# Performance work log

Hardware: AMD Instinct MI355X
Metric: run time of the kernel (lower is better)

Reference implementation:

```python
import jax, jax.numpy as jnp
import numpy as np

B, D, N = 256, 256, 100000
NUM_CLUSTERS, NUM_CLASSES = 100, 1000


def setup_inputs() -> dict:
    key = jax.random.key(0)
    k1, k2, k3, k4, k5, k6 = jax.random.split(key, 6)
    return {
        "feature": jax.random.normal(k1, (B, D), dtype=jnp.float32),
        "feature_bank": jax.random.normal(k2, (N, D), dtype=jnp.float32),
        "cluster_label_bank": jax.random.randint(k3, (N,), 0, NUM_CLUSTERS, dtype=jnp.int64)
            if jax.config.jax_enable_x64 else jax.random.randint(k3, (N,), 0, NUM_CLUSTERS).astype(jnp.int32),
        "class_label_bank": jax.random.randint(k4, (N,), 0, NUM_CLASSES).astype(jnp.int32),
        "cluster_idx": jax.random.randint(k5, (B,), 0, NUM_CLUSTERS).astype(jnp.int32),
        "gt_label": jax.random.randint(k6, (B,), 0, NUM_CLASSES).astype(jnp.int32),
    }


def reference(feature, feature_bank, cluster_label_bank, class_label_bank, cluster_idx, gt_label):
    # Masks: primary = same cluster AND different class; fallback = different class only.
    cluster_label_bank = cluster_label_bank.astype(jnp.int32)
    same_cluster = cluster_label_bank[None, :] == cluster_idx[:, None].astype(jnp.int32)  # [B, N]
    diff_class = class_label_bank[None, :] != gt_label[:, None]                            # [B, N]
    mask_primary = same_cluster & diff_class
    has_primary = mask_primary.any(axis=1, keepdims=True)
    mask = jnp.where(has_primary, mask_primary, diff_class)  # [B, N]

    # Euclidean distances (torch.cdist p=2): ||a-b|| via expanded squared form.
    a2 = jnp.sum(feature * feature, axis=1)[:, None]              # [B, 1]
    b2 = jnp.sum(feature_bank * feature_bank, axis=1)[None, :]    # [1, N]
    d2 = a2 + b2 - 2.0 * (feature @ feature_bank.T)               # [B, N]
    dist = jnp.sqrt(jnp.maximum(d2, 0.0))

    # Masked argmin over the bank, then gather negatives.
    dist_masked = jnp.where(mask, dist, jnp.inf)
    neg_idx = jnp.argmin(dist_masked, axis=1)                     # [B]
    negatives = feature_bank[neg_idx]                             # [B, D]
    return negatives
```

## Files before the change

kernel.cpp:

```cpp
#include <hip/hip_runtime.h>
#include <climits>

typedef __attribute__((ext_vector_type(8))) short s8;
typedef __attribute__((ext_vector_type(4))) float f32x4;

#define BQ    256
#define DDIM  256
#define NBANK 100000
#define BN    64
#define NJB   ((NBANK + BN - 1) / BN)
#define SENT  1e30f

__device__ inline void splitElem(float x, s8& h, s8& l, int i) {
    unsigned u  = __float_as_uint(x);
    unsigned uh = (u + 0x8000u) & 0xFFFF0000u;
    h[i] = (short)(uh >> 16);
    float lf = x - __uint_as_float(uh);
    l[i] = (short)((__float_as_uint(lf) + 0x8000u) >> 16);
}

__device__ inline void split8(const float4 v0, const float4 v1, s8& h, s8& l) {
    splitElem(v0.x, h, l, 0); splitElem(v0.y, h, l, 1);
    splitElem(v0.z, h, l, 2); splitElem(v0.w, h, l, 3);
    splitElem(v1.x, h, l, 4); splitElem(v1.y, h, l, 5);
    splitElem(v1.z, h, l, 6); splitElem(v1.w, h, l, 7);
}

__device__ inline float sq8(const float4 v0, const float4 v1, float s) {
    s = fmaf(v0.x, v0.x, s); s = fmaf(v0.y, v0.y, s);
    s = fmaf(v0.z, v0.z, s); s = fmaf(v0.w, v0.w, s);
    s = fmaf(v1.x, v1.x, s); s = fmaf(v1.y, v1.y, s);
    s = fmaf(v1.z, v1.z, s); s = fmaf(v1.w, v1.w, s);
    return s;
}

__device__ inline unsigned fkey(float f) {
    unsigned u = __float_as_uint(f);
    return u ^ (((int)u < 0) ? 0xFFFFFFFFu : 0x80000000u);
}

__global__ __launch_bounds__(512) void split_feature(
    const float* __restrict__ feature, s8* __restrict__ fH, s8* __restrict__ fL)
{
    const int t    = blockIdx.x * 512 + threadIdx.x;
    const int lane = t & 63, ks = (t >> 6) & 7, rt = t >> 9;
    const int row  = rt * 16 + (lane & 15);
    const int k0   = ks * 32 + (lane >> 4) * 8;
    const float* p = feature + (size_t)row * DDIM + k0;
    const float4 v0 = *(const float4*)p;
    const float4 v1 = *(const float4*)(p + 4);
    s8 h, l;
    split8(v0, v1, h, l);
    fH[t] = h; fL[t] = l;
}

__global__ __launch_bounds__(512, 4) void gemm_argmin_msplit(
    const s8* __restrict__ fH, const s8* __restrict__ fL,
    const float* __restrict__ bank,
    const int* __restrict__ cluster_label, const int* __restrict__ class_label,
    const int* __restrict__ cluster_idx,  const int* __restrict__ gt_label,
    unsigned long long* __restrict__ wsP, unsigned long long* __restrict__ wsD)
{
    __shared__ __align__(16) s8 bHs[4 * 4 * 64];
    __shared__ __align__(16) s8 bLs[4 * 4 * 64];
    __shared__ float b2s[BN];
    __shared__ int clsS[BN], cluS[BN], rowGt[128], rowClu[128];

    const int tid = threadIdx.x;
    const int bb  = blockIdx.x;
    const int jb  = bb >> 1, mh = bb & 1;
    const int j0  = jb * BN;
    const int r0  = mh * 128;

    const int col = tid >> 3, q = tid & 7;
    const int ct_s = col >> 4, cl_s = col & 15;
    const int sl_s = q >> 1, p_s = q & 1;
    const int w = tid >> 6, lane = tid & 63;
    const int g = lane >> 4, c = lane & 15;

    int jcol = j0 + col; if (jcol >= NBANK) jcol = NBANK - 1;
    const float* gb = bank + (size_t)jcol * DDIM + q * 16;

    if (tid < 128) {
        rowGt[tid]  = gt_label[r0 + tid];
        rowClu[tid] = cluster_idx[r0 + tid];
    }
    if (tid < BN) {
        int jg = j0 + tid; int jc = jg < NBANK ? jg : NBANK - 1;
        clsS[tid] = class_label[jc];
        cluS[tid] = cluster_label[jc];
    }
    float4 a0 = *(const float4*)(gb);
    float4 a1 = *(const float4*)(gb + 4);
    float4 a2 = *(const float4*)(gb + 8);
    float4 a3 = *(const float4*)(gb + 12);

    float sqa = 0.f;
    {
        s8 h, l;
        split8(a0, a1, h, l);
        sqa = sq8(a0, a1, sqa);
        int wi = (((sl_s * 4 + ct_s) * 64 + (p_s * 2 + 0) * 16 + cl_s)) ^ q;
        bHs[wi] = h; bLs[wi] = l;
        split8(a2, a3, h, l);
        sqa = sq8(a2, a3, sqa);
        wi = (((sl_s * 4 + ct_s) * 64 + (p_s * 2 + 1) * 16 + cl_s)) ^ q;
        bHs[wi] = h; bLs[wi] = l;
    }
    __syncthreads();

    a0 = *(const float4*)(gb + 128);
    a1 = *(const float4*)(gb + 132);
    a2 = *(const float4*)(gb + 136);
    a3 = *(const float4*)(gb + 140);

    f32x4 acc[4];
    #pragma unroll
    for (int ct = 0; ct < 4; ++ct)
        acc[ct] = (f32x4){0.f, 0.f, 0.f, 0.f};

    const int RT = mh * 8 + w;

    #pragma unroll
    for (int sl = 0; sl < 4; ++sl) {
        const s8 aH = fH[(RT * 8 + sl) * 64 + lane];
        const s8 aL = fL[(RT * 8 + sl) * 64 + lane];
        const int rx = sl * 2 + (lane >> 5);
        #pragma unroll
        for (int ct = 0; ct < 4; ++ct) {
            const s8 bh = bHs[((sl * 4 + ct) * 64 + lane) ^ rx];
            const s8 bl = bLs[((sl * 4 + ct) * 64 + lane) ^ rx];
            acc[ct] = __builtin_amdgcn_mfma_f32_16x16x32_bf16(aH, bh, acc[ct], 0, 0, 0);
            acc[ct] = __builtin_amdgcn_mfma_f32_16x16x32_bf16(aH, bl, acc[ct], 0, 0, 0);
            acc[ct] = __builtin_amdgcn_mfma_f32_16x16x32_bf16(aL, bh, acc[ct], 0, 0, 0);
        }
    }
    __syncthreads();

    {
        s8 h, l;
        split8(a0, a1, h, l);
        sqa = sq8(a0, a1, sqa);
        int wi = (((sl_s * 4 + ct_s) * 64 + (p_s * 2 + 0) * 16 + cl_s)) ^ q;
        bHs[wi] = h; bLs[wi] = l;
        split8(a2, a3, h, l);
        sqa = sq8(a2, a3, sqa);
        wi = (((sl_s * 4 + ct_s) * 64 + (p_s * 2 + 1) * 16 + cl_s)) ^ q;
        bHs[wi] = h; bLs[wi] = l;
    }
    sqa += __shfl_xor(sqa, 1);
    sqa += __shfl_xor(sqa, 2);
    sqa += __shfl_xor(sqa, 4);
    if (q == 0) b2s[col] = sqa;
    __syncthreads();

    #pragma unroll
    for (int sl = 0; sl < 4; ++sl) {
        const s8 aH = fH[(RT * 8 + 4 + sl) * 64 + lane];
        const s8 aL = fL[(RT * 8 + 4 + sl) * 64 + lane];
        const int rx = sl * 2 + (lane >> 5);
        #pragma unroll
        for (int ct = 0; ct < 4; ++ct) {
            const s8 bh = bHs[((sl * 4 + ct) * 64 + lane) ^ rx];
            const s8 bl = bLs[((sl * 4 + ct) * 64 + lane) ^ rx];
            acc[ct] = __builtin_amdgcn_mfma_f32_16x16x32_bf16(aH, bh, acc[ct], 0, 0, 0);
            acc[ct] = __builtin_amdgcn_mfma_f32_16x16x32_bf16(aH, bl, acc[ct], 0, 0, 0);
            acc[ct] = __builtin_amdgcn_mfma_f32_16x16x32_bf16(aL, bh, acc[ct], 0, 0, 0);
        }
    }

    #pragma unroll
    for (int r = 0; r < 4; ++r) {
        const int lrow = w * 16 + g * 4 + r;
        const int myGt = rowGt[lrow], myClu = rowClu[lrow];
        unsigned long long pk = ~0ull, dk = ~0ull;
        #pragma unroll
        for (int ct = 0; ct < 4; ++ct) {
            const int jg = j0 + ct * 16 + c;
            const float sc = b2s[ct * 16 + c] - 2.f * acc[ct][r];
            if (jg < NBANK && clsS[ct * 16 + c] != myGt) {
                const unsigned long long k =
                    ((unsigned long long)fkey(sc) << 32) | (unsigned)jg;
                dk = k < dk ? k : dk;
                if (cluS[ct * 16 + c] == myClu) pk = k < pk ? k : pk;
            }
        }
        #pragma unroll
        for (int off = 1; off < 16; off <<= 1) {
            unsigned long long ok = __shfl_xor(pk, off);
            pk = ok < pk ? ok : pk;
            ok = __shfl_xor(dk, off);
            dk = ok < dk ? ok : dk;
        }
        if (c == 0) {
            const size_t o = (size_t)jb * BQ + r0 + lrow;
            wsP[o] = pk;
            wsD[o] = dk;
        }
    }
}

__global__ __launch_bounds__(256) void reduce_gather(
    const unsigned long long* __restrict__ wsP,
    const unsigned long long* __restrict__ wsD,
    const float* __restrict__ bank, float* __restrict__ out)
{
    const int row = blockIdx.x, tid = threadIdx.x;
    unsigned long long pk = ~0ull, dk = ~0ull;
    for (int b = tid; b < NJB; b += 256) {
        unsigned long long k = wsP[(size_t)b * BQ + row];
        pk = k < pk ? k : pk;
        k = wsD[(size_t)b * BQ + row];
        dk = k < dk ? k : dk;
    }
    #pragma unroll
    for (int off = 32; off > 0; off >>= 1) {
        unsigned long long ok = __shfl_down(pk, off);
        pk = ok < pk ? ok : pk;
        ok = __shfl_down(dk, off);
        dk = ok < dk ? ok : dk;
    }
    __shared__ unsigned long long swP[4], swD[4];
    __shared__ int sIdx;
    const int lane = tid & 63, wv = tid >> 6;
    if (lane == 0) { swP[wv] = pk; swD[wv] = dk; }
    __syncthreads();
    if (tid == 0) {
        unsigned long long p = swP[0], d = swD[0];
        #pragma unroll
        for (int k2 = 1; k2 < 4; ++k2) {
            p = swP[k2] < p ? swP[k2] : p;
            d = swD[k2] < d ? swD[k2] : d;
        }
        sIdx = (p != ~0ull) ? (int)(unsigned)(p & 0xFFFFFFFFull)
             : ((d != ~0ull) ? (int)(unsigned)(d & 0xFFFFFFFFull) : 0);
    }
    __syncthreads();
    out[(size_t)row * DDIM + tid] = bank[(size_t)sIdx * DDIM + tid];
}

extern "C" void kernel_launch(void* const* d_in, const int* in_sizes, int n_in,
                              void* d_out, int out_size, void* d_ws, size_t ws_size,
                              hipStream_t stream) {
    const float* feature       = (const float*)d_in[0];
    const float* bank          = (const float*)d_in[1];
    const int*   cluster_label = (const int*)d_in[2];
    const int*   class_label   = (const int*)d_in[3];
    const int*   cluster_idx   = (const int*)d_in[4];
    const int*   gt_label      = (const int*)d_in[5];
    float* out = (float*)d_out;

    s8* fH = (s8*)d_ws;
    s8* fL = fH + 8192;
    unsigned long long* wsP = (unsigned long long*)((char*)d_ws + 2 * 8192 * sizeof(s8));
    unsigned long long* wsD = wsP + (size_t)BQ * NJB;

    hipLaunchKernelGGL(split_feature, dim3(16), dim3(512), 0, stream, feature, fH, fL);
    hipLaunchKernelGGL(gemm_argmin_msplit, dim3(NJB * 2), dim3(512), 0, stream,
                       fH, fL, bank, cluster_label, class_label, cluster_idx, gt_label,
                       wsP, wsD);
    hipLaunchKernelGGL(reduce_gather, dim3(BQ), dim3(256), 0, stream,
                       wsP, wsD, bank, out);
}
```

Before: 217.8 us.

## Process two bank column tiles per block with cross-tile prefetch

Each GEMM block now handles 128 bank columns as two consecutive 64-column tiles instead of one. The global loads for the next tile are issued before the current tile's MFMA work, so memory latency overlaps compute across tile boundaries. This also halves the number of blocks and the partial-result workspace that the reduction kernel scans. The cost is longer serial work per block and fewer blocks, which may reduce load balance across CUs.

```diff
diff --git a/kernel.cpp b/kernel.cpp
--- a/kernel.cpp
+++ b/kernel.cpp
@@ -9,6 +9,7 @@
 #define NBANK 100000
 #define BN    64
 #define NJB   ((NBANK + BN - 1) / BN)
+#define NJB2  ((NJB + 1) / 2)
 #define SENT  1e30f
 
 __device__ inline void splitElem(float x, s8& h, s8& l, int i) {
@@ -54,7 +55,7 @@
     fH[t] = h; fL[t] = l;
 }
 
-__global__ __launch_bounds__(512, 4) void gemm_argmin_msplit(
+__global__ __launch_bounds__(512, 4) void gemm_argmin_2t(
     const s8* __restrict__ fH, const s8* __restrict__ fL,
     const float* __restrict__ bank,
     const int* __restrict__ cluster_label, const int* __restrict__ class_label,
@@ -63,13 +64,13 @@
 {
     __shared__ __align__(16) s8 bHs[4 * 4 * 64];
     __shared__ __align__(16) s8 bLs[4 * 4 * 64];
-    __shared__ float b2s[BN];
-    __shared__ int clsS[BN], cluS[BN], rowGt[128], rowClu[128];
+    __shared__ float b2s[128];
+    __shared__ int clsS[128], cluS[128], rowGt[128], rowClu[128];
 
     const int tid = threadIdx.x;
     const int bb  = blockIdx.x;
-    const int jb  = bb >> 1, mh = bb & 1;
-    const int j0  = jb * BN;
+    const int jb2 = bb >> 1, mh = bb & 1;
+    const int j0  = jb2 * 128;
     const int r0  = mh * 128;
 
     const int col = tid >> 3, q = tid & 7;
@@ -77,98 +78,83 @@
     const int sl_s = q >> 1, p_s = q & 1;
     const int w = tid >> 6, lane = tid & 63;
     const int g = lane >> 4, c = lane & 15;
-
-    int jcol = j0 + col; if (jcol >= NBANK) jcol = NBANK - 1;
-    const float* gb = bank + (size_t)jcol * DDIM + q * 16;
+    const int RT = mh * 8 + w;
+
+    int jc0 = j0 + col;      if (jc0 >= NBANK) jc0 = NBANK - 1;
+    int jc1 = j0 + 64 + col; if (jc1 >= NBANK) jc1 = NBANK - 1;
+    const float* gb0 = bank + (size_t)jc0 * DDIM + q * 16;
+    const float* gb1 = bank + (size_t)jc1 * DDIM + q * 16;
 
     if (tid < 128) {
         rowGt[tid]  = gt_label[r0 + tid];
         rowClu[tid] = cluster_idx[r0 + tid];
-    }
-    if (tid < BN) {
         int jg = j0 + tid; int jc = jg < NBANK ? jg : NBANK - 1;
         clsS[tid] = class_label[jc];
         cluS[tid] = cluster_label[jc];
     }
-    float4 a0 = *(const float4*)(gb);
-    float4 a1 = *(const float4*)(gb + 4);
-    float4 a2 = *(const float4*)(gb + 8);
-    float4 a3 = *(const float4*)(gb + 12);
+    float4 a0 = *(const float4*)(gb0);
+    float4 a1 = *(const float4*)(gb0 + 4);
+    float4 a2 = *(const float4*)(gb0 + 8);
+    float4 a3 = *(const float4*)(gb0 + 12);
+
+#define STAGE(SQA)                                                             \
+    {                                                                          \
+        s8 h_, l_;                                                             \
+        split8(a0, a1, h_, l_);                                                \
+        SQA = sq8(a0, a1, SQA);                                                \
+        int wi_ = (((sl_s * 4 + ct_s) * 64 + (p_s * 2 + 0) * 16 + cl_s)) ^ q;  \
+        bHs[wi_] = h_; bLs[wi_] = l_;                                          \
+        split8(a2, a3, h_, l_);                                                \
+        SQA = sq8(a2, a3, SQA);                                                \
+        wi_ = (((sl_s * 4 + ct_s) * 64 + (p_s * 2 + 1) * 16 + cl_s)) ^ q;      \
+        bHs[wi_] = h_; bLs[wi_] = l_;                                          \
+    }
+
+#define LOADA(PTR, OFF)                                                        \
+    a0 = *(const float4*)((PTR) + (OFF));                                      \
+    a1 = *(const float4*)((PTR) + (OFF) + 4);                                  \
+    a2 = *(const float4*)((PTR) + (OFF) + 8);                                  \
+    a3 = *(const float4*)((PTR) + (OFF) + 12);
+
+#define COMPUTE(HBASE)                                                         \
+    _Pragma("unroll")                                                          \
+    for (int sl = 0; sl < 4; ++sl) {                                           \
+        const s8 aH = fH[(RT * 8 + (HBASE) + sl) * 64 + lane];                 \
+        const s8 aL = fL[(RT * 8 + (HBASE) + sl) * 64 + lane];                 \
+        const int rx = sl * 2 + (lane >> 5);                                   \
+        _Pragma("unroll")                                                      \
+        for (int ct = 0; ct < 4; ++ct) {                                       \
+            const s8 bh = bHs[((sl * 4 + ct) * 64 + lane) ^ rx];               \
+            const s8 bl = bLs[((sl * 4 + ct) * 64 + lane) ^ rx];               \
+            acc[ct] = __builtin_amdgcn_mfma_f32_16x16x32_bf16(aH, bh, acc[ct], 0, 0, 0); \
+            acc[ct] = __builtin_amdgcn_mfma_f32_16x16x32_bf16(aH, bl, acc[ct], 0, 0, 0); \
+            acc[ct] = __builtin_amdgcn_mfma_f32_16x16x32_bf16(aL, bh, acc[ct], 0, 0, 0); \
+        }                                                                      \
+    }
+
+    f32x4 acc[4];
+    unsigned long long pkA[4], dkA[4];
 
     float sqa = 0.f;
-    {
-        s8 h, l;
-        split8(a0, a1, h, l);
-        sqa = sq8(a0, a1, sqa);
-        int wi = (((sl_s * 4 + ct_s) * 64 + (p_s * 2 + 0) * 16 + cl_s)) ^ q;
-        bHs[wi] = h; bLs[wi] = l;
-        split8(a2, a3, h, l);
-        sqa = sq8(a2, a3, sqa);
-        wi = (((sl_s * 4 + ct_s) * 64 + (p_s * 2 + 1) * 16 + cl_s)) ^ q;
-        bHs[wi] = h; bLs[wi] = l;
-    }
-    __syncthreads();
-
-    a0 = *(const float4*)(gb + 128);
-    a1 = *(const float4*)(gb + 132);
-    a2 = *(const float4*)(gb + 136);
-    a3 = *(const float4*)(gb + 140);
-
-    f32x4 acc[4];
-    #pragma unroll
-    for (int ct = 0; ct < 4; ++ct)
-        acc[ct] = (f32x4){0.f, 0.f, 0.f, 0.f};
-
-    const int RT = mh * 8 + w;
-
-    #pragma unroll
-    for (int sl = 0; sl < 4; ++sl) {
-        const s8 aH = fH[(RT * 8 + sl) * 64 + lane];
-        const s8 aL = fL[(RT * 8 + sl) * 64 + lane];
-        const int rx = sl * 2 + (lane >> 5);
-        #pragma unroll
-        for (int ct = 0; ct < 4; ++ct) {
-            const s8 bh = bHs[((sl * 4 + ct) * 64 + lane) ^ rx];
-            const s8 bl = bLs[((sl * 4 + ct) * 64 + lane) ^ rx];
-            acc[ct] = __builtin_amdgcn_mfma_f32_16x16x32_bf16(aH, bh, acc[ct], 0, 0, 0);
-            acc[ct] = __builtin_amdgcn_mfma_f32_16x16x32_bf16(aH, bl, acc[ct], 0, 0, 0);
-            acc[ct] = __builtin_amdgcn_mfma_f32_16x16x32_bf16(aL, bh, acc[ct], 0, 0, 0);
-        }
-    }
-    __syncthreads();
-
-    {
-        s8 h, l;
-        split8(a0, a1, h, l);
-        sqa = sq8(a0, a1, sqa);
-        int wi = (((sl_s * 4 + ct_s) * 64 + (p_s * 2 + 0) * 16 + cl_s)) ^ q;
-        bHs[wi] = h; bLs[wi] = l;
-        split8(a2, a3, h, l);
-        sqa = sq8(a2, a3, sqa);
-        wi = (((sl_s * 4 + ct_s) * 64 + (p_s * 2 + 1) * 16 + cl_s)) ^ q;
-        bHs[wi] = h; bLs[wi] = l;
-    }
+    STAGE(sqa);
+    __syncthreads();
+    LOADA(gb0, 128);
+    #pragma unroll
+    for (int ct = 0; ct < 4; ++ct) acc[ct] = (f32x4){0.f, 0.f, 0.f, 0.f};
+    COMPUTE(0);
+    __syncthreads();
+    STAGE(sqa);
     sqa += __shfl_xor(sqa, 1);
     sqa += __shfl_xor(sqa, 2);
     sqa += __shfl_xor(sqa, 4);
     if (q == 0) b2s[col] = sqa;
     __syncthreads();
-
-    #pragma unroll
-    for (int sl = 0; sl < 4; ++sl) {
-        const s8 aH = fH[(RT * 8 + 4 + sl) * 64 + lane];
-        const s8 aL = fL[(RT * 8 + 4 + sl) * 64 + lane];
-        const int rx = sl * 2 + (lane >> 5);
-        #pragma unroll
-        for (int ct = 0; ct < 4; ++ct) {
-            const s8 bh = bHs[((sl * 4 + ct) * 64 + lane) ^ rx];
-            const s8 bl = bLs[((sl * 4 + ct) * 64 + lane) ^ rx];
-            acc[ct] = __builtin_amdgcn_mfma_f32_16x16x32_bf16(aH, bh, acc[ct], 0, 0, 0);
-            acc[ct] = __builtin_amdgcn_mfma_f32_16x16x32_bf16(aH, bl, acc[ct], 0, 0, 0);
-            acc[ct] = __builtin_amdgcn_mfma_f32_16x16x32_bf16(aL, bh, acc[ct], 0, 0, 0);
-        }
-    }
-
+    LOADA(gb1, 0);
+    COMPUTE(4);
+    __syncthreads();
+
+    sqa = 0.f;
+    STAGE(sqa);
     #pragma unroll
     for (int r = 0; r < 4; ++r) {
         const int lrow = w * 16 + g * 4 + r;
@@ -176,13 +162,48 @@
         unsigned long long pk = ~0ull, dk = ~0ull;
         #pragma unroll
         for (int ct = 0; ct < 4; ++ct) {
-            const int jg = j0 + ct * 16 + c;
-            const float sc = b2s[ct * 16 + c] - 2.f * acc[ct][r];
-            if (jg < NBANK && clsS[ct * 16 + c] != myGt) {
+            const int li = ct * 16 + c;
+            const int jg = j0 + li;
+            const float sc = b2s[li] - 2.f * acc[ct][r];
+            if (jg < NBANK && clsS[li] != myGt) {
                 const unsigned long long k =
                     ((unsigned long long)fkey(sc) << 32) | (unsigned)jg;
                 dk = k < dk ? k : dk;
-                if (cluS[ct * 16 + c] == myClu) pk = k < pk ? k : pk;
+                if (cluS[li] == myClu) pk = k < pk ? k : pk;
+            }
+        }
+        pkA[r] = pk; dkA[r] = dk;
+    }
+    __syncthreads();
+
+    LOADA(gb1, 128);
+    #pragma unroll
+    for (int ct = 0; ct < 4; ++ct) acc[ct] = (f32x4){0.f, 0.f, 0.f, 0.f};
+    COMPUTE(0);
+    __syncthreads();
+    STAGE(sqa);
+    sqa += __shfl_xor(sqa, 1);
+    sqa += __shfl_xor(sqa, 2);
+    sqa += __shfl_xor(sqa, 4);
+    if (q == 0) b2s[64 + col] = sqa;
+    __syncthreads();
+    COMPUTE(4);
+
+    #pragma unroll
+    for (int r = 0; r < 4; ++r) {
+        const int lrow = w * 16 + g * 4 + r;
+        const int myGt = rowGt[lrow], myClu = rowClu[lrow];
+        unsigned long long pk = pkA[r], dk = dkA[r];
+        #pragma unroll
+        for (int ct = 0; ct < 4; ++ct) {
+            const int li = 64 + ct * 16 + c;
+            const int jg = j0 + li;
+            const float sc = b2s[li] - 2.f * acc[ct][r];
+            if (jg < NBANK && clsS[li] != myGt) {
+                const unsigned long long k =
+                    ((unsigned long long)fkey(sc) << 32) | (unsigned)jg;
+                dk = k < dk ? k : dk;
+                if (cluS[li] == myClu) pk = k < pk ? k : pk;
             }
         }
         #pragma unroll
@@ -193,11 +214,14 @@
             dk = ok < dk ? ok : dk;
         }
         if (c == 0) {
-            const size_t o = (size_t)jb * BQ + r0 + lrow;
+            const size_t o = (size_t)jb2 * BQ + r0 + lrow;
             wsP[o] = pk;
             wsD[o] = dk;
         }
     }
+#undef STAGE
+#undef LOADA
+#undef COMPUTE
 }
 
 __global__ __launch_bounds__(256) void reduce_gather(
@@ -207,7 +231,7 @@
 {
     const int row = blockIdx.x, tid = threadIdx.x;
     unsigned long long pk = ~0ull, dk = ~0ull;
-    for (int b = tid; b < NJB; b += 256) {
+    for (int b = tid; b < NJB2; b += 256) {
         unsigned long long k = wsP[(size_t)b * BQ + row];
         pk = k < pk ? k : pk;
         k = wsD[(size_t)b * BQ + row];
@@ -253,10 +277,10 @@
     s8* fH = (s8*)d_ws;
     s8* fL = fH + 8192;
     unsigned long long* wsP = (unsigned long long*)((char*)d_ws + 2 * 8192 * sizeof(s8));
-    unsigned long long* wsD = wsP + (size_t)BQ * NJB;
+    unsigned long long* wsD = wsP + (size_t)BQ * NJB2;
 
     hipLaunchKernelGGL(split_feature, dim3(16), dim3(512), 0, stream, feature, fH, fL);
-    hipLaunchKernelGGL(gemm_argmin_msplit, dim3(NJB * 2), dim3(512), 0, stream,
+    hipLaunchKernelGGL(gemm_argmin_2t, dim3(NJB2 * 2), dim3(512), 0, stream,
                        fH, fL, bank, cluster_label, class_label, cluster_idx, gt_label,
                        wsP, wsD);
     hipLaunchKernelGGL(reduce_gather, dim3(BQ), dim3(256), 0, stream,
```

Result: no change. 214.9 us (-1.3%).

## Cover all 256 query rows per block with 1024 threads instead of splitting M

Applied to the files above, without the earlier changes.

Each block previously handled half of the query rows, so every bank tile was loaded from global memory, split into bf16 hi/lo and squared twice, once per M-half. Now one 1024-thread block covers all 256 rows for its 64-column bank tile, so each bank element is loaded and converted only once, with each thread handling 8 floats per phase. The cost is fewer, larger blocks: occupancy limits under launch_bounds(1024,4) and fewer independent blocks to hide latency may offset the halved bank traffic.

```diff
diff --git a/kernel.cpp b/kernel.cpp
--- a/kernel.cpp
+++ b/kernel.cpp
@@ -54,7 +54,7 @@
     fH[t] = h; fL[t] = l;
 }
 
-__global__ __launch_bounds__(512, 4) void gemm_argmin_msplit(
+__global__ __launch_bounds__(1024, 4) void gemm_argmin_fullm(
     const s8* __restrict__ fH, const s8* __restrict__ fL,
     const float* __restrict__ bank,
     const int* __restrict__ cluster_label, const int* __restrict__ class_label,
@@ -64,26 +64,24 @@
     __shared__ __align__(16) s8 bHs[4 * 4 * 64];
     __shared__ __align__(16) s8 bLs[4 * 4 * 64];
     __shared__ float b2s[BN];
-    __shared__ int clsS[BN], cluS[BN], rowGt[128], rowClu[128];
+    __shared__ int clsS[BN], cluS[BN], rowGt[BQ], rowClu[BQ];
 
     const int tid = threadIdx.x;
-    const int bb  = blockIdx.x;
-    const int jb  = bb >> 1, mh = bb & 1;
+    const int jb  = blockIdx.x;
     const int j0  = jb * BN;
-    const int r0  = mh * 128;
-
-    const int col = tid >> 3, q = tid & 7;
+
+    const int col = tid >> 4, q = tid & 15;
     const int ct_s = col >> 4, cl_s = col & 15;
-    const int sl_s = q >> 1, p_s = q & 1;
+    const int sl_s = q >> 2, o_s = q & 3;
     const int w = tid >> 6, lane = tid & 63;
     const int g = lane >> 4, c = lane & 15;
 
     int jcol = j0 + col; if (jcol >= NBANK) jcol = NBANK - 1;
-    const float* gb = bank + (size_t)jcol * DDIM + q * 16;
-
-    if (tid < 128) {
-        rowGt[tid]  = gt_label[r0 + tid];
-        rowClu[tid] = cluster_idx[r0 + tid];
+    const float* gb = bank + (size_t)jcol * DDIM + q * 8;
+
+    if (tid < BQ) {
+        rowGt[tid]  = gt_label[tid];
+        rowClu[tid] = cluster_idx[tid];
     }
     if (tid < BN) {
         int jg = j0 + tid; int jc = jg < NBANK ? jg : NBANK - 1;
@@ -92,40 +90,30 @@
     }
     float4 a0 = *(const float4*)(gb);
     float4 a1 = *(const float4*)(gb + 4);
-    float4 a2 = *(const float4*)(gb + 8);
-    float4 a3 = *(const float4*)(gb + 12);
 
     float sqa = 0.f;
     {
         s8 h, l;
         split8(a0, a1, h, l);
         sqa = sq8(a0, a1, sqa);
-        int wi = (((sl_s * 4 + ct_s) * 64 + (p_s * 2 + 0) * 16 + cl_s)) ^ q;
-        bHs[wi] = h; bLs[wi] = l;
-        split8(a2, a3, h, l);
-        sqa = sq8(a2, a3, sqa);
-        wi = (((sl_s * 4 + ct_s) * 64 + (p_s * 2 + 1) * 16 + cl_s)) ^ q;
+        const int wi = (((sl_s * 4 + ct_s) * 64 + o_s * 16 + cl_s)) ^ q;
         bHs[wi] = h; bLs[wi] = l;
     }
     __syncthreads();
 
     a0 = *(const float4*)(gb + 128);
     a1 = *(const float4*)(gb + 132);
-    a2 = *(const float4*)(gb + 136);
-    a3 = *(const float4*)(gb + 140);
 
     f32x4 acc[4];
     #pragma unroll
     for (int ct = 0; ct < 4; ++ct)
         acc[ct] = (f32x4){0.f, 0.f, 0.f, 0.f};
 
-    const int RT = mh * 8 + w;
-
     #pragma unroll
     for (int sl = 0; sl < 4; ++sl) {
-        const s8 aH = fH[(RT * 8 + sl) * 64 + lane];
-        const s8 aL = fL[(RT * 8 + sl) * 64 + lane];
-        const int rx = sl * 2 + (lane >> 5);
+        const s8 aH = fH[(w * 8 + sl) * 64 + lane];
+        const s8 aL = fL[(w * 8 + sl) * 64 + lane];
+        const int rx = sl * 4 + g;
         #pragma unroll
         for (int ct = 0; ct < 4; ++ct) {
             const s8 bh = bHs[((sl * 4 + ct) * 64 + lane) ^ rx];
@@ -141,24 +129,21 @@
         s8 h, l;
         split8(a0, a1, h, l);
         sqa = sq8(a0, a1, sqa);
-        int wi = (((sl_s * 4 + ct_s) * 64 + (p_s * 2 + 0) * 16 + cl_s)) ^ q;
-        bHs[wi] = h; bLs[wi] = l;
-        split8(a2, a3, h, l);
-        sqa = sq8(a2, a3, sqa);
-        wi = (((sl_s * 4 + ct_s) * 64 + (p_s * 2 + 1) * 16 + cl_s)) ^ q;
+        const int wi = (((sl_s * 4 + ct_s) * 64 + o_s * 16 + cl_s)) ^ q;
         bHs[wi] = h; bLs[wi] = l;
     }
     sqa += __shfl_xor(sqa, 1);
     sqa += __shfl_xor(sqa, 2);
     sqa += __shfl_xor(sqa, 4);
+    sqa += __shfl_xor(sqa, 8);
     if (q == 0) b2s[col] = sqa;
     __syncthreads();
 
     #pragma unroll
     for (int sl = 0; sl < 4; ++sl) {
-        const s8 aH = fH[(RT * 8 + 4 + sl) * 64 + lane];
-        const s8 aL = fL[(RT * 8 + 4 + sl) * 64 + lane];
-        const int rx = sl * 2 + (lane >> 5);
+        const s8 aH = fH[(w * 8 + 4 + sl) * 64 + lane];
+        const s8 aL = fL[(w * 8 + 4 + sl) * 64 + lane];
+        const int rx = sl * 4 + g;
         #pragma unroll
         for (int ct = 0; ct < 4; ++ct) {
             const s8 bh = bHs[((sl * 4 + ct) * 64 + lane) ^ rx];
@@ -171,18 +156,19 @@
 
     #pragma unroll
     for (int r = 0; r < 4; ++r) {
-        const int lrow = w * 16 + g * 4 + r;
-        const int myGt = rowGt[lrow], myClu = rowClu[lrow];
+        const int row  = w * 16 + g * 4 + r;
+        const int myGt = rowGt[row], myClu = rowClu[row];
         unsigned long long pk = ~0ull, dk = ~0ull;
         #pragma unroll
         for (int ct = 0; ct < 4; ++ct) {
-            const int jg = j0 + ct * 16 + c;
-            const float sc = b2s[ct * 16 + c] - 2.f * acc[ct][r];
-            if (jg < NBANK && clsS[ct * 16 + c] != myGt) {
+            const int li = ct * 16 + c;
+            const int jg = j0 + li;
+            const float sc = b2s[li] - 2.f * acc[ct][r];
+            if (jg < NBANK && clsS[li] != myGt) {
                 const unsigned long long k =
                     ((unsigned long long)fkey(sc) << 32) | (unsigned)jg;
                 dk = k < dk ? k : dk;
-                if (cluS[ct * 16 + c] == myClu) pk = k < pk ? k : pk;
+                if (cluS[li] == myClu) pk = k < pk ? k : pk;
             }
         }
         #pragma unroll
@@ -193,7 +179,7 @@
             dk = ok < dk ? ok : dk;
         }
         if (c == 0) {
-            const size_t o = (size_t)jb * BQ + r0 + lrow;
+            const size_t o = (size_t)jb * BQ + row;
             wsP[o] = pk;
             wsD[o] = dk;
         }
@@ -256,7 +242,7 @@
     unsigned long long* wsD = wsP + (size_t)BQ * NJB;
 
     hipLaunchKernelGGL(split_feature, dim3(16), dim3(512), 0, stream, feature, fH, fL);
-    hipLaunchKernelGGL(gemm_argmin_msplit, dim3(NJB * 2), dim3(512), 0, stream,
+    hipLaunchKernelGGL(gemm_argmin_fullm, dim3(NJB), dim3(1024), 0, stream,
                        fH, fL, bank, cluster_label, class_label, cluster_idx, gt_label,
                        wsP, wsD);
     hipLaunchKernelGGL(reduce_gather, dim3(BQ), dim3(256), 0, stream,
```

Measured after the change: 218.2 us. No clear change (+0.2%).

## Cover all 256 query rows per block so each bank tile is split once

Applied to the files above, without the earlier changes.

Drops the two-way split over query rows. Each block now processes all 256 feature rows against its 64-column bank tile, with every wave computing two 16-row tiles. Before, the two row halves each loaded the same bank tile from global memory and converted it to bf16 hi/lo, so this removes that duplicated load and split work and halves the grid. In exchange each wave holds twice the accumulators, which raises register pressure and may lower occupancy under launch_bounds(512,4), and there are fewer blocks to spread across CUs.

```diff
diff --git a/kernel.cpp b/kernel.cpp
--- a/kernel.cpp
+++ b/kernel.cpp
@@ -54,7 +54,7 @@
     fH[t] = h; fL[t] = l;
 }
 
-__global__ __launch_bounds__(512, 4) void gemm_argmin_msplit(
+__global__ __launch_bounds__(512, 4) void gemm_argmin_rt2(
     const s8* __restrict__ fH, const s8* __restrict__ fL,
     const float* __restrict__ bank,
     const int* __restrict__ cluster_label, const int* __restrict__ class_label,
@@ -64,13 +64,11 @@
     __shared__ __align__(16) s8 bHs[4 * 4 * 64];
     __shared__ __align__(16) s8 bLs[4 * 4 * 64];
     __shared__ float b2s[BN];
-    __shared__ int clsS[BN], cluS[BN], rowGt[128], rowClu[128];
+    __shared__ int clsS[BN], cluS[BN], rowGt[BQ], rowClu[BQ];
 
     const int tid = threadIdx.x;
-    const int bb  = blockIdx.x;
-    const int jb  = bb >> 1, mh = bb & 1;
+    const int jb  = blockIdx.x;
     const int j0  = jb * BN;
-    const int r0  = mh * 128;
 
     const int col = tid >> 3, q = tid & 7;
     const int ct_s = col >> 4, cl_s = col & 15;
@@ -81,9 +79,9 @@
     int jcol = j0 + col; if (jcol >= NBANK) jcol = NBANK - 1;
     const float* gb = bank + (size_t)jcol * DDIM + q * 16;
 
-    if (tid < 128) {
-        rowGt[tid]  = gt_label[r0 + tid];
-        rowClu[tid] = cluster_idx[r0 + tid];
+    if (tid < BQ) {
+        rowGt[tid]  = gt_label[tid];
+        rowClu[tid] = cluster_idx[tid];
     }
     if (tid < BN) {
         int jg = j0 + tid; int jc = jg < NBANK ? jg : NBANK - 1;
@@ -114,25 +112,33 @@
     a2 = *(const float4*)(gb + 136);
     a3 = *(const float4*)(gb + 140);
 
-    f32x4 acc[4];
+    f32x4 acc[4][2];
     #pragma unroll
     for (int ct = 0; ct < 4; ++ct)
-        acc[ct] = (f32x4){0.f, 0.f, 0.f, 0.f};
-
-    const int RT = mh * 8 + w;
+        #pragma unroll
+        for (int rt = 0; rt < 2; ++rt)
+            acc[ct][rt] = (f32x4){0.f, 0.f, 0.f, 0.f};
 
     #pragma unroll
     for (int sl = 0; sl < 4; ++sl) {
-        const s8 aH = fH[(RT * 8 + sl) * 64 + lane];
-        const s8 aL = fL[(RT * 8 + sl) * 64 + lane];
+        s8 aH[2], aL[2];
+        #pragma unroll
+        for (int rt = 0; rt < 2; ++rt) {
+            const int RT = w * 2 + rt;
+            aH[rt] = fH[(RT * 8 + sl) * 64 + lane];
+            aL[rt] = fL[(RT * 8 + sl) * 64 + lane];
+        }
         const int rx = sl * 2 + (lane >> 5);
         #pragma unroll
         for (int ct = 0; ct < 4; ++ct) {
             const s8 bh = bHs[((sl * 4 + ct) * 64 + lane) ^ rx];
             const s8 bl = bLs[((sl * 4 + ct) * 64 + lane) ^ rx];
-            acc[ct] = __builtin_amdgcn_mfma_f32_16x16x32_bf16(aH, bh, acc[ct], 0, 0, 0);
-            acc[ct] = __builtin_amdgcn_mfma_f32_16x16x32_bf16(aH, bl, acc[ct], 0, 0, 0);
-            acc[ct] = __builtin_amdgcn_mfma_f32_16x16x32_bf16(aL, bh, acc[ct], 0, 0, 0);
+            #pragma unroll
+            for (int rt = 0; rt < 2; ++rt) {
+                acc[ct][rt] = __builtin_amdgcn_mfma_f32_16x16x32_bf16(aH[rt], bh, acc[ct][rt], 0, 0, 0);
+                acc[ct][rt] = __builtin_amdgcn_mfma_f32_16x16x32_bf16(aH[rt], bl, acc[ct][rt], 0, 0, 0);
+                acc[ct][rt] = __builtin_amdgcn_mfma_f32_16x16x32_bf16(aL[rt], bh, acc[ct][rt], 0, 0, 0);
+            }
         }
     }
     __syncthreads();
@@ -156,46 +162,58 @@
 
     #pragma unroll
     for (int sl = 0; sl < 4; ++sl) {
-        const s8 aH = fH[(RT * 8 + 4 + sl) * 64 + lane];
-        const s8 aL = fL[(RT * 8 + 4 + sl) * 64 + lane];
+        s8 aH[2], aL[2];
+        #pragma unroll
+        for (int rt = 0; rt < 2; ++rt) {
+            const int RT = w * 2 + rt;
+            aH[rt] = fH[(RT * 8 + 4 + sl) * 64 + lane];
+            aL[rt] = fL[(RT * 8 + 4 + sl) * 64 + lane];
+        }
         const int rx = sl * 2 + (lane >> 5);
         #pragma unroll
         for (int ct = 0; ct < 4; ++ct) {
             const s8 bh = bHs[((sl * 4 + ct) * 64 + lane) ^ rx];
             const s8 bl = bLs[((sl * 4 + ct) * 64 + lane) ^ rx];
-            acc[ct] = __builtin_amdgcn_mfma_f32_16x16x32_bf16(aH, bh, acc[ct], 0, 0, 0);
-            acc[ct] = __builtin_amdgcn_mfma_f32_16x16x32_bf16(aH, bl, acc[ct], 0, 0, 0);
-            acc[ct] = __builtin_amdgcn_mfma_f32_16x16x32_bf16(aL, bh, acc[ct], 0, 0, 0);
-        }
-    }
-
-    #pragma unroll
-    for (int r = 0; r < 4; ++r) {
-        const int lrow = w * 16 + g * 4 + r;
-        const int myGt = rowGt[lrow], myClu = rowClu[lrow];
-        unsigned long long pk = ~0ull, dk = ~0ull;
-        #pragma unroll
-        for (int ct = 0; ct < 4; ++ct) {
-            const int jg = j0 + ct * 16 + c;
-            const float sc = b2s[ct * 16 + c] - 2.f * acc[ct][r];
-            if (jg < NBANK && clsS[ct * 16 + c] != myGt) {
-                const unsigned long long k =
-                    ((unsigned long long)fkey(sc) << 32) | (unsigned)jg;
-                dk = k < dk ? k : dk;
-                if (cluS[ct * 16 + c] == myClu) pk = k < pk ? k : pk;
-            }
-        }
-        #pragma unroll
-        for (int off = 1; off < 16; off <<= 1) {
-            unsigned long long ok = __shfl_xor(pk, off);
-            pk = ok < pk ? ok : pk;
-            ok = __shfl_xor(dk, off);
-            dk = ok < dk ? ok : dk;
-        }
-        if (c == 0) {
-            const size_t o = (size_t)jb * BQ + r0 + lrow;
-            wsP[o] = pk;
-            wsD[o] = dk;
+            #pragma unroll
+            for (int rt = 0; rt < 2; ++rt) {
+                acc[ct][rt] = __builtin_amdgcn_mfma_f32_16x16x32_bf16(aH[rt], bh, acc[ct][rt], 0, 0, 0);
+                acc[ct][rt] = __builtin_amdgcn_mfma_f32_16x16x32_bf16(aH[rt], bl, acc[ct][rt], 0, 0, 0);
+                acc[ct][rt] = __builtin_amdgcn_mfma_f32_16x16x32_bf16(aL[rt], bh, acc[ct][rt], 0, 0, 0);
+            }
+        }
+    }
+
+    #pragma unroll
+    for (int rt = 0; rt < 2; ++rt) {
+        #pragma unroll
+        for (int r = 0; r < 4; ++r) {
+            const int row  = w * 32 + rt * 16 + g * 4 + r;
+            const int myGt = rowGt[row], myClu = rowClu[row];
+            unsigned long long pk = ~0ull, dk = ~0ull;
+            #pragma unroll
+            for (int ct = 0; ct < 4; ++ct) {
+                const int li = ct * 16 + c;
+                const int jg = j0 + li;
+                const float sc = b2s[li] - 2.f * acc[ct][rt][r];
+                if (jg < NBANK && clsS[li] != myGt) {
+                    const unsigned long long k =
+                        ((unsigned long long)fkey(sc) << 32) | (unsigned)jg;
+                    dk = k < dk ? k : dk;
+                    if (cluS[li] == myClu) pk = k < pk ? k : pk;
+                }
+            }
+            #pragma unroll
+            for (int off = 1; off < 16; off <<= 1) {
+                unsigned long long ok = __shfl_xor(pk, off);
+                pk = ok < pk ? ok : pk;
+                ok = __shfl_xor(dk, off);
+                dk = ok < dk ? ok : dk;
+            }
+            if (c == 0) {
+                const size_t o = (size_t)jb * BQ + row;
+                wsP[o] = pk;
+                wsD[o] = dk;
+            }
         }
     }
 }
@@ -256,7 +274,7 @@
     unsigned long long* wsD = wsP + (size_t)BQ * NJB;
 
     hipLaunchKernelGGL(split_feature, dim3(16), dim3(512), 0, stream, feature, fH, fL);
-    hipLaunchKernelGGL(gemm_argmin_msplit, dim3(NJB * 2), dim3(512), 0, stream,
+    hipLaunchKernelGGL(gemm_argmin_rt2, dim3(NJB), dim3(512), 0, stream,
                        fH, fL, bank, cluster_label, class_label, cluster_idx, gt_label,
                        wsP, wsD);
     hipLaunchKernelGGL(reduce_gather, dim3(BQ), dim3(256), 0, stream,
```

Result: faster. 212.2 us (-2.6%).
